# Optimization experiments

Hardware: AMD Instinct MI355X
Metric: run time of the kernel (lower is better)

Reference implementation:

```python
import jax, jax.numpy as jnp
import numpy as np
from jax import lax

H = W = 512          # frame size (n_dim_x, n_dim_y)
K = 3                # kernel_size
C_IN, C1, C2 = 3, 20, 40
N_ACT = 18           # YarsRevenge action space
H1, W1 = H - (K - 1), W - (K - 1)   # 510 conv1 output
H2, W2 = H1 - (K - 1), W1 - (K - 1) # 508 conv2 output


def conv2d(x, w, b):
    # valid NCHW conv, same as nn.Conv2d with no padding
    y = lax.conv_general_dilated(x, w, (1, 1), 'VALID',
                                 dimension_numbers=('NCHW', 'OIHW', 'NCHW'))
    return y + b[None, :, None, None]


def setup_inputs() -> dict:
    key = jax.random.key(0)
    ks = jax.random.split(key, 8)
    x_prev = jax.random.normal(ks[0], (1, C_IN, H, W), jnp.float32)
    # current frame differs from previous only in a localized patch (RL frame diff)
    patch = jax.random.normal(ks[1], (1, C_IN, 48, 64), jnp.float32)
    x = x_prev.at[:, :, 120:168, 200:264].add(patch)
    conv1_w = jax.random.normal(ks[2], (C1, C_IN, K, K), jnp.float32) * 0.05
    conv1_b = jax.random.normal(ks[3], (C1,), jnp.float32) * 0.05
    conv2_w = jax.random.normal(ks[4], (C2, C1, K, K), jnp.float32) * 0.05
    conv2_b = jax.random.normal(ks[5], (C2,), jnp.float32) * 0.05
    fc_w = jax.random.normal(ks[6], (N_ACT, C2 * H2 * W2), jnp.float32) * 1e-3
    # cached activations from the first (full) forward pass on x_prev
    last_c1 = jax.nn.relu(conv2d(x_prev, conv1_w, conv1_b))
    last_c2 = jax.nn.relu(conv2d(last_c1, conv2_w, conv2_b))
    return dict(x=x, x_prev=x_prev, last_c1=last_c1, last_c2=last_c2,
                conv1_w=conv1_w, conv1_b=conv1_b,
                conv2_w=conv2_w, conv2_b=conv2_b, fc_w=fc_w)


def _min_max(mask_1d, n):
    idx = jnp.arange(n)
    mn = jnp.min(jnp.where(mask_1d, idx, n))
    mx = jnp.max(jnp.where(mask_1d, idx, -1))
    return mn, mx


def reference(x, x_prev, last_c1, last_c2, conv1_w, conv1_b, conv2_w, conv2_b, fc_w):
    # --- bounding box of changed pixels (torch: x_diff.nonzero(), min/max) ---
    diff = jnp.any((x_prev - x) != 0, axis=(0, 1))   # [H, W]
    mn_x, mx_x = _min_max(jnp.any(diff, axis=1), H)
    mn_y, mx_y = _min_max(jnp.any(diff, axis=0), W)
    r_x1 = jnp.maximum(mn_x - (K - 1), 0)
    r_x2 = jnp.minimum(mx_x + K, H)
    r_y1 = jnp.maximum(mn_y - (K - 1), 0)
    r_y2 = jnp.minimum(mx_y + K, W)

    # Valid conv of the slice [r1:r2] equals the full conv restricted to output
    # rows [r1, r2-(K-1)); we express the dynamic-shape gather-conv-scatter as a
    # full conv + masked blend (identical math, jit-compatible static shapes).
    i1 = jnp.arange(H1)
    rows1 = (i1 >= r_x1) & (i1 < r_x2 - (K - 1))
    cols1 = (i1 >= r_y1) & (i1 < r_y2 - (K - 1))
    mask1 = rows1[:, None] & cols1[None, :]
    c1_full = jax.nn.relu(conv2d(x, conv1_w, conv1_b))
    c1 = jnp.where(mask1, c1_full, last_c1)

    # expand region for second conv (torch clamps slice ends implicitly to c1 size)
    rb_x1 = jnp.maximum(r_x1 - (K - 1), 0)
    rb_x2 = jnp.minimum(jnp.minimum(r_x2 + K, H), H1)
    rb_y1 = jnp.maximum(r_y1 - (K - 1), 0)
    rb_y2 = jnp.minimum(jnp.minimum(r_y2 + K, W), W1)
    i2 = jnp.arange(H2)
    rows2 = (i2 >= rb_x1) & (i2 < rb_x2 - (K - 1))
    cols2 = (i2 >= rb_y1) & (i2 < rb_y2 - (K - 1))
    mask2 = rows2[:, None] & cols2[None, :]
    c2_full = jax.nn.relu(conv2d(c1, conv2_w, conv2_b))
    c2 = jnp.where(mask2, c2_full, last_c2)

    logits = fc_w @ c2.reshape(-1)   # bias-free Linear
    return jax.nn.softmax(logits, axis=-1)
```

## Files before the change

### kernel.cpp

```cpp
#include <hip/hip_runtime.h>
#include <cfloat>

#define Hh 512
#define Ww 512
#define H1 510
#define W1 510
#define H2 508
#define W2 508
#define CIN 3
#define C1C 20
#define C2C 40
#define NACT 18
#define NFC (C2C * H2 * W2)
#define N4  (NFC / 4)

#define GRID_MV   2048
#define GRID_CORR 256

struct Box { int rx1, rx2, ry1, ry2, bx1, bx2, by1, by2; };

__device__ inline Box make_box(const int* __restrict__ bb) {
  Box b;
  int mnx = bb[0], mxx = bb[1], mny = bb[2], mxy = bb[3];
  b.rx1 = max(mnx - 2, 0);  b.rx2 = min(mxx + 3, Hh);
  b.ry1 = max(mny - 2, 0);  b.ry2 = min(mxy + 3, Ww);
  b.bx1 = max(b.rx1 - 2, 0); b.bx2 = min(min(b.rx2 + 3, Hh), H1);
  b.by1 = max(b.ry1 - 2, 0); b.by2 = min(min(b.ry2 + 3, Ww), W1);
  return b;
}

__global__ void k_init(int* __restrict__ bbox) {
  bbox[0] = Hh; bbox[1] = -1; bbox[2] = Ww; bbox[3] = -1;
}

__global__ __launch_bounds__(256) void k_bbox(const float* __restrict__ x,
                                              const float* __restrict__ xp,
                                              int* __restrict__ bbox) {
  int idx = blockIdx.x * 256 + threadIdx.x;
  int h = idx >> 9, w = idx & 511;
  bool d = false;
#pragma unroll
  for (int c = 0; c < CIN; ++c)
    d |= (x[c * Hh * Ww + idx] != xp[c * Hh * Ww + idx]);
  int hmin = d ? h : 0x7FFFFFFF;
  int hmax = d ? h : -1;
  int wmin = d ? w : 0x7FFFFFFF;
  int wmax = d ? w : -1;
#pragma unroll
  for (int off = 32; off > 0; off >>= 1) {
    hmin = min(hmin, __shfl_down(hmin, off, 64));
    hmax = max(hmax, __shfl_down(hmax, off, 64));
    wmin = min(wmin, __shfl_down(wmin, off, 64));
    wmax = max(wmax, __shfl_down(wmax, off, 64));
  }
  if ((threadIdx.x & 63) == 0 && hmax >= 0) {
    atomicMin(&bbox[0], hmin);
    atomicMax(&bbox[1], hmax);
    atomicMin(&bbox[2], wmin);
    atomicMax(&bbox[3], wmax);
  }
}

__global__ __launch_bounds__(256) void k_c1(const float* __restrict__ x,
                                            const float* __restrict__ w1,
                                            const float* __restrict__ b1,
                                            const float* __restrict__ lc1,
                                            const int* __restrict__ bbox,
                                            float* __restrict__ c1buf) {
  Box b = make_box(bbox);
  int R1h = b.bx2 - b.bx1, R1w = b.by2 - b.by1;
  if (R1h <= 0 || R1w <= 0) return;
  int total = C1C * R1h * R1w;
  int m1r1 = b.rx2 - 2, m1c1 = b.ry2 - 2;
  int stride = gridDim.x * blockDim.x;
  for (int e = blockIdx.x * blockDim.x + threadIdx.x; e < total; e += stride) {
    int c = e / (R1h * R1w);
    int rem = e - c * (R1h * R1w);
    int ri = rem / R1w;
    int rj = rem - ri * R1w;
    int i = b.bx1 + ri, j = b.by1 + rj;
    float val;
    if (i >= b.rx1 && i < m1r1 && j >= b.ry1 && j < m1c1) {
      float s = b1[c];
#pragma unroll
      for (int ic = 0; ic < CIN; ++ic)
#pragma unroll
        for (int kh = 0; kh < 3; ++kh)
#pragma unroll
          for (int kw = 0; kw < 3; ++kw)
            s = fmaf(x[(ic * Hh + i + kh) * Ww + j + kw],
                     w1[((c * CIN + ic) * 3 + kh) * 3 + kw], s);
      val = fmaxf(s, 0.f);
    } else {
      val = lc1[(c * H1 + i) * W1 + j];
    }
    c1buf[e] = val;
  }
}

__global__ __launch_bounds__(256) void k_c2(const float* __restrict__ c1buf,
                                            const float* __restrict__ w2,
                                            const float* __restrict__ b2,
                                            const float* __restrict__ lc2,
                                            const int* __restrict__ bbox,
                                            float* __restrict__ delta) {
  Box b = make_box(bbox);
  int R1h = b.bx2 - b.bx1, R1w = b.by2 - b.by1;
  int R2h = R1h - 2, R2w = R1w - 2;
  if (R2h <= 0 || R2w <= 0) return;
  int total = C2C * R2h * R2w;
  int stride = gridDim.x * blockDim.x;
  for (int e = blockIdx.x * blockDim.x + threadIdx.x; e < total; e += stride) {
    int oc = e / (R2h * R2w);
    int rem = e - oc * (R2h * R2w);
    int ri = rem / R2w;
    int rj = rem - ri * R2w;
    int i2 = b.bx1 + ri, j2 = b.by1 + rj;
    float s = b2[oc];
#pragma unroll 4
    for (int ic = 0; ic < C1C; ++ic)
#pragma unroll
      for (int kh = 0; kh < 3; ++kh)
#pragma unroll
        for (int kw = 0; kw < 3; ++kw)
          s = fmaf(c1buf[(ic * R1h + ri + kh) * R1w + rj + kw],
                   w2[((oc * C1C + ic) * 3 + kh) * 3 + kw], s);
    float val = fmaxf(s, 0.f);
    delta[e] = val - lc2[(oc * H2 + i2) * W2 + j2];
  }
}

__device__ inline void block_reduce_store(float* acc, float* __restrict__ partial) {
#pragma unroll
  for (int a = 0; a < NACT; ++a)
#pragma unroll
    for (int off = 32; off > 0; off >>= 1)
      acc[a] += __shfl_down(acc[a], off, 64);
  __shared__ float red[4][NACT];
  int lane = threadIdx.x & 63, wid = threadIdx.x >> 6;
  if (lane == 0) {
#pragma unroll
    for (int a = 0; a < NACT; ++a) red[wid][a] = acc[a];
  }
  __syncthreads();
  if (threadIdx.x < NACT) {
    float s = red[0][threadIdx.x] + red[1][threadIdx.x] +
              red[2][threadIdx.x] + red[3][threadIdx.x];
    partial[blockIdx.x * NACT + threadIdx.x] = s;
  }
}

__global__ __launch_bounds__(256) void k_mv(const float4* __restrict__ fcw,
                                            const float4* __restrict__ vec,
                                            float* __restrict__ partial1) {
  float acc[NACT];
#pragma unroll
  for (int a = 0; a < NACT; ++a) acc[a] = 0.f;
  int stride = gridDim.x * blockDim.x;
  for (int col = blockIdx.x * blockDim.x + threadIdx.x; col < N4; col += stride) {
    float4 v = vec[col];
#pragma unroll
    for (int a = 0; a < NACT; ++a) {
      float4 w = fcw[(size_t)a * N4 + col];
      acc[a] += w.x * v.x + w.y * v.y + w.z * v.z + w.w * v.w;
    }
  }
  block_reduce_store(acc, partial1);
}

__global__ __launch_bounds__(256) void k_corr(const float* __restrict__ fcw,
                                              const float* __restrict__ delta,
                                              const int* __restrict__ bbox,
                                              float* __restrict__ partial2) {
  Box b = make_box(bbox);
  int R1h = b.bx2 - b.bx1, R1w = b.by2 - b.by1;
  int R2h = R1h - 2, R2w = R1w - 2;
  int total = (R2h > 0 && R2w > 0) ? C2C * R2h * R2w : 0;
  float acc[NACT];
#pragma unroll
  for (int a = 0; a < NACT; ++a) acc[a] = 0.f;
  int stride = gridDim.x * blockDim.x;
  for (int e = blockIdx.x * blockDim.x + threadIdx.x; e < total; e += stride) {
    int oc = e / (R2h * R2w);
    int rem = e - oc * (R2h * R2w);
    int ri = rem / R2w;
    int rj = rem - ri * R2w;
    int gidx = (oc * H2 + b.bx1 + ri) * W2 + b.by1 + rj;
    float d = delta[e];
#pragma unroll
    for (int a = 0; a < NACT; ++a)
      acc[a] = fmaf(fcw[(size_t)a * NFC + gidx], d, acc[a]);
  }
  block_reduce_store(acc, partial2);
}

__global__ __launch_bounds__(1024) void k_final(const float* __restrict__ partial1,
                                                const float* __restrict__ partial2,
                                                float* __restrict__ out) {
  __shared__ float red[1024];
  __shared__ float logits[NACT];
  int t = threadIdx.x;
  float s = 0.f;
  const int NG = 1024 / NACT;
  if (t < NG * NACT) {
    int a = t % NACT, g = t / NACT;
    for (int bi = g; bi < GRID_MV; bi += NG)   s += partial1[bi * NACT + a];
    for (int bi = g; bi < GRID_CORR; bi += NG) s += partial2[bi * NACT + a];
  }
  red[t] = s;
  __syncthreads();
  if (t < NACT) {
    float tot = 0.f;
    for (int g = 0; g < NG; ++g) tot += red[g * NACT + t];
    logits[t] = tot;
  }
  __syncthreads();
  if (t == 0) {
    float mx = -FLT_MAX;
#pragma unroll
    for (int a = 0; a < NACT; ++a) mx = fmaxf(mx, logits[a]);
    float se = 0.f;
    float e[NACT];
#pragma unroll
    for (int a = 0; a < NACT; ++a) { e[a] = expf(logits[a] - mx); se += e[a]; }
    float inv = 1.f / se;
#pragma unroll
    for (int a = 0; a < NACT; ++a) out[a] = e[a] * inv;
  }
}

extern "C" void kernel_launch(void* const* d_in, const int* in_sizes, int n_in,
                              void* d_out, int out_size, void* d_ws, size_t ws_size,
                              hipStream_t stream) {
  const float* x   = (const float*)d_in[0];
  const float* xp  = (const float*)d_in[1];
  const float* lc1 = (const float*)d_in[2];
  const float* lc2 = (const float*)d_in[3];
  const float* w1  = (const float*)d_in[4];
  const float* b1  = (const float*)d_in[5];
  const float* w2  = (const float*)d_in[6];
  const float* b2  = (const float*)d_in[7];
  const float* fcw = (const float*)d_in[8];
  float* out = (float*)d_out;

  char* ws = (char*)d_ws;
  int*   bbox     = (int*)ws;
  float* partial1 = (float*)(ws + 1024);
  float* partial2 = (float*)(ws + 1024 + 147456);
  size_t off_c1 = 262144, off_dl = 1048576;
  if (ws_size >= ((size_t)96 << 20)) { off_c1 = (size_t)8 << 20; off_dl = (size_t)40 << 20; }
  float* c1buf = (float*)(ws + off_c1);
  float* delta = (float*)(ws + off_dl);

  k_init<<<1, 1, 0, stream>>>(bbox);
  k_bbox<<<1024, 256, 0, stream>>>(x, xp, bbox);
  k_c1<<<64, 256, 0, stream>>>(x, w1, b1, lc1, bbox, c1buf);
  k_c2<<<128, 256, 0, stream>>>(c1buf, w2, b2, lc2, bbox, delta);
  k_mv<<<GRID_MV, 256, 0, stream>>>((const float4*)fcw, (const float4*)lc2, partial1);
  k_corr<<<GRID_CORR, 256, 0, stream>>>(fcw, delta, bbox, partial2);
  k_final<<<1, 1024, 0, stream>>>(partial1, partial2, out);
}
```

Measured before the change: 1.059 ms.

## Fuse conv2 with FC correction, vectorize bbox, chunk the FC matvec with nontemporal loads

Merges the conv2 kernel and the FC correction kernel so the conv2 delta is consumed in registers, with no delta buffer written and read back. The bbox diff scan now loads float4 and uses bitmask ffs/clz to find column extents. The large FC matvec over the cached conv2 activations now gives each block a contiguous chunk, uses nontemporal loads for the weights, and is launched first. Main cost remains streaming the roughly 186 MB FC weight, which bounds the total.

```diff
diff --git a/kernel.cpp b/kernel.cpp
--- a/kernel.cpp
+++ b/kernel.cpp
@@ -1,5 +1,6 @@
 #include <hip/hip_runtime.h>
 #include <cfloat>
+#include <climits>
 
 #define Hh 512
 #define Ww 512
@@ -15,7 +16,9 @@
 #define N4  (NFC / 4)
 
 #define GRID_MV   2048
-#define GRID_CORR 256
+#define GRID_C2   256
+
+typedef float f32x4 __attribute__((ext_vector_type(4)));
 
 struct Box { int rx1, rx2, ry1, ry2, bx1, bx2, by1, by2; };
 
@@ -33,19 +36,26 @@
   bbox[0] = Hh; bbox[1] = -1; bbox[2] = Ww; bbox[3] = -1;
 }
 
-__global__ __launch_bounds__(256) void k_bbox(const float* __restrict__ x,
-                                              const float* __restrict__ xp,
+__global__ __launch_bounds__(256) void k_bbox(const f32x4* __restrict__ x4,
+                                              const f32x4* __restrict__ xp4,
                                               int* __restrict__ bbox) {
-  int idx = blockIdx.x * 256 + threadIdx.x;
-  int h = idx >> 9, w = idx & 511;
-  bool d = false;
-#pragma unroll
-  for (int c = 0; c < CIN; ++c)
-    d |= (x[c * Hh * Ww + idx] != xp[c * Hh * Ww + idx]);
-  int hmin = d ? h : 0x7FFFFFFF;
-  int hmax = d ? h : -1;
-  int wmin = d ? w : 0x7FFFFFFF;
-  int wmax = d ? w : -1;
+  int q = blockIdx.x * 256 + threadIdx.x;
+  int h = q >> 7, w0 = (q & 127) << 2;
+  unsigned dm = 0;
+#pragma unroll
+  for (int c = 0; c < CIN; ++c) {
+    f32x4 a = x4[c * 65536 + q], b = xp4[c * 65536 + q];
+    dm |= (a.x != b.x) ? 1u : 0u;
+    dm |= (a.y != b.y) ? 2u : 0u;
+    dm |= (a.z != b.z) ? 4u : 0u;
+    dm |= (a.w != b.w) ? 8u : 0u;
+  }
+  int hmin = dm ? h : INT_MAX, hmax = dm ? h : -1;
+  int wmin = INT_MAX, wmax = -1;
+  if (dm) {
+    wmin = w0 + (__ffs(dm) - 1);
+    wmax = w0 + (31 - __clz(dm));
+  }
 #pragma unroll
   for (int off = 32; off > 0; off >>= 1) {
     hmin = min(hmin, __shfl_down(hmin, off, 64));
@@ -98,38 +108,6 @@
   }
 }
 
-__global__ __launch_bounds__(256) void k_c2(const float* __restrict__ c1buf,
-                                            const float* __restrict__ w2,
-                                            const float* __restrict__ b2,
-                                            const float* __restrict__ lc2,
-                                            const int* __restrict__ bbox,
-                                            float* __restrict__ delta) {
-  Box b = make_box(bbox);
-  int R1h = b.bx2 - b.bx1, R1w = b.by2 - b.by1;
-  int R2h = R1h - 2, R2w = R1w - 2;
-  if (R2h <= 0 || R2w <= 0) return;
-  int total = C2C * R2h * R2w;
-  int stride = gridDim.x * blockDim.x;
-  for (int e = blockIdx.x * blockDim.x + threadIdx.x; e < total; e += stride) {
-    int oc = e / (R2h * R2w);
-    int rem = e - oc * (R2h * R2w);
-    int ri = rem / R2w;
-    int rj = rem - ri * R2w;
-    int i2 = b.bx1 + ri, j2 = b.by1 + rj;
-    float s = b2[oc];
-#pragma unroll 4
-    for (int ic = 0; ic < C1C; ++ic)
-#pragma unroll
-      for (int kh = 0; kh < 3; ++kh)
-#pragma unroll
-        for (int kw = 0; kw < 3; ++kw)
-          s = fmaf(c1buf[(ic * R1h + ri + kh) * R1w + rj + kw],
-                   w2[((oc * C1C + ic) * 3 + kh) * 3 + kw], s);
-    float val = fmaxf(s, 0.f);
-    delta[e] = val - lc2[(oc * H2 + i2) * W2 + j2];
-  }
-}
-
 __device__ inline void block_reduce_store(float* acc, float* __restrict__ partial) {
 #pragma unroll
   for (int a = 0; a < NACT; ++a)
@@ -150,28 +128,13 @@
   }
 }
 
-__global__ __launch_bounds__(256) void k_mv(const float4* __restrict__ fcw,
-                                            const float4* __restrict__ vec,
-                                            float* __restrict__ partial1) {
-  float acc[NACT];
-#pragma unroll
-  for (int a = 0; a < NACT; ++a) acc[a] = 0.f;
-  int stride = gridDim.x * blockDim.x;
-  for (int col = blockIdx.x * blockDim.x + threadIdx.x; col < N4; col += stride) {
-    float4 v = vec[col];
-#pragma unroll
-    for (int a = 0; a < NACT; ++a) {
-      float4 w = fcw[(size_t)a * N4 + col];
-      acc[a] += w.x * v.x + w.y * v.y + w.z * v.z + w.w * v.w;
-    }
-  }
-  block_reduce_store(acc, partial1);
-}
-
-__global__ __launch_bounds__(256) void k_corr(const float* __restrict__ fcw,
-                                              const float* __restrict__ delta,
-                                              const int* __restrict__ bbox,
-                                              float* __restrict__ partial2) {
+__global__ __launch_bounds__(256) void k_c2corr(const float* __restrict__ c1buf,
+                                                const float* __restrict__ w2,
+                                                const float* __restrict__ b2,
+                                                const float* __restrict__ lc2,
+                                                const float* __restrict__ fcw,
+                                                const int* __restrict__ bbox,
+                                                float* __restrict__ partial2) {
   Box b = make_box(bbox);
   int R1h = b.bx2 - b.bx1, R1w = b.by2 - b.by1;
   int R2h = R1h - 2, R2w = R1w - 2;
@@ -185,13 +148,42 @@
     int rem = e - oc * (R2h * R2w);
     int ri = rem / R2w;
     int rj = rem - ri * R2w;
+    float s = b2[oc];
+#pragma unroll 4
+    for (int ic = 0; ic < C1C; ++ic)
+#pragma unroll
+      for (int kh = 0; kh < 3; ++kh)
+#pragma unroll
+        for (int kw = 0; kw < 3; ++kw)
+          s = fmaf(c1buf[(ic * R1h + ri + kh) * R1w + rj + kw],
+                   w2[((oc * C1C + ic) * 3 + kh) * 3 + kw], s);
     int gidx = (oc * H2 + b.bx1 + ri) * W2 + b.by1 + rj;
-    float d = delta[e];
+    float d = fmaxf(s, 0.f) - lc2[gidx];
 #pragma unroll
     for (int a = 0; a < NACT; ++a)
       acc[a] = fmaf(fcw[(size_t)a * NFC + gidx], d, acc[a]);
   }
   block_reduce_store(acc, partial2);
+}
+
+__global__ __launch_bounds__(256) void k_mv(const f32x4* __restrict__ fcw,
+                                            const f32x4* __restrict__ vec,
+                                            float* __restrict__ partial1) {
+  const int CHUNK = (N4 + GRID_MV - 1) / GRID_MV;
+  int start = blockIdx.x * CHUNK;
+  int end = min(start + CHUNK, N4);
+  float acc[NACT];
+#pragma unroll
+  for (int a = 0; a < NACT; ++a) acc[a] = 0.f;
+  for (int col = start + threadIdx.x; col < end; col += 256) {
+    f32x4 v = vec[col];
+#pragma unroll
+    for (int a = 0; a < NACT; ++a) {
+      f32x4 w = __builtin_nontemporal_load(&fcw[(size_t)a * N4 + col]);
+      acc[a] += w.x * v.x + w.y * v.y + w.z * v.z + w.w * v.w;
+    }
+  }
+  block_reduce_store(acc, partial1);
 }
 
 __global__ __launch_bounds__(1024) void k_final(const float* __restrict__ partial1,
@@ -204,8 +196,8 @@
   const int NG = 1024 / NACT;
   if (t < NG * NACT) {
     int a = t % NACT, g = t / NACT;
-    for (int bi = g; bi < GRID_MV; bi += NG)   s += partial1[bi * NACT + a];
-    for (int bi = g; bi < GRID_CORR; bi += NG) s += partial2[bi * NACT + a];
+    for (int bi = g; bi < GRID_MV; bi += NG) s += partial1[bi * NACT + a];
+    for (int bi = g; bi < GRID_C2; bi += NG) s += partial2[bi * NACT + a];
   }
   red[t] = s;
   __syncthreads();
@@ -245,18 +237,14 @@
 
   char* ws = (char*)d_ws;
   int*   bbox     = (int*)ws;
-  float* partial1 = (float*)(ws + 1024);
-  float* partial2 = (float*)(ws + 1024 + 147456);
-  size_t off_c1 = 262144, off_dl = 1048576;
-  if (ws_size >= ((size_t)96 << 20)) { off_c1 = (size_t)8 << 20; off_dl = (size_t)40 << 20; }
-  float* c1buf = (float*)(ws + off_c1);
-  float* delta = (float*)(ws + off_dl);
-
+  float* partial1 = (float*)(ws + 4096);
+  float* partial2 = (float*)(ws + 4096 + 147456);
+  float* c1buf    = (float*)(ws + (1u << 20));
+
+  k_mv<<<GRID_MV, 256, 0, stream>>>((const f32x4*)fcw, (const f32x4*)lc2, partial1);
   k_init<<<1, 1, 0, stream>>>(bbox);
-  k_bbox<<<1024, 256, 0, stream>>>(x, xp, bbox);
+  k_bbox<<<256, 256, 0, stream>>>((const f32x4*)x, (const f32x4*)xp, bbox);
   k_c1<<<64, 256, 0, stream>>>(x, w1, b1, lc1, bbox, c1buf);
-  k_c2<<<128, 256, 0, stream>>>(c1buf, w2, b2, lc2, bbox, delta);
-  k_mv<<<GRID_MV, 256, 0, stream>>>((const float4*)fcw, (const float4*)lc2, partial1);
-  k_corr<<<GRID_CORR, 256, 0, stream>>>(fcw, delta, bbox, partial2);
+  k_c2corr<<<GRID_C2, 256, 0, stream>>>(c1buf, w2, b2, lc2, fcw, bbox, partial2);
   k_final<<<1, 1024, 0, stream>>>(partial1, partial2, out);
 }
```

Result: faster. 1.028 ms (-2.9%).
